# Kernel tuning notes

Hardware: AMD Instinct MI355X
Metric: run time of the kernel (lower is better)

Reference implementation:

```python
import jax, jax.numpy as jnp
import numpy as np

N_HEADS = 16
LN_EPS = 1e-5


def setup_inputs() -> dict:
    key = jax.random.key(0)
    k_z, k_qkv, k_proj = jax.random.split(key, 3)
    b, n, dm = 4, 2048, 1024
    z = jax.random.normal(k_z, (b, n, dm), dtype=jnp.float32)
    gamma = jnp.ones((dm,), dtype=jnp.float32)
    beta = jnp.zeros((dm,), dtype=jnp.float32)
    # parameterize Linear weights as (in, out) so y = x @ w (same math as torch x @ W.T)
    w_qkv = jax.random.normal(k_qkv, (dm, 3 * dm), dtype=jnp.float32) * (1.0 / np.sqrt(dm))
    w_proj = jax.random.normal(k_proj, (dm, dm), dtype=jnp.float32) * (1.0 / np.sqrt(dm))
    b_proj = jnp.zeros((dm,), dtype=jnp.float32)
    return {"z": z, "gamma": gamma, "beta": beta, "w_qkv": w_qkv,
            "w_proj": w_proj, "b_proj": b_proj}


def reference(z, gamma, beta, w_qkv, w_proj, b_proj):
    b, n, dm = z.shape
    h = N_HEADS
    d = dm // h
    scaling = jnp.asarray(np.sqrt(dm / h), dtype=z.dtype)

    # LayerNorm over last dim
    mu = jnp.mean(z, axis=-1, keepdims=True)
    var = jnp.mean(jnp.square(z - mu), axis=-1, keepdims=True)
    zn = (z - mu) * jax.lax.rsqrt(var + LN_EPS) * gamma + beta

    qkv = zn @ w_qkv  # [b, n, 3*dm]
    # einops 'b n (h d qkv_n) -> qkv_n b h n d': qkv index is INNERMOST of packed dim
    qkv = qkv.reshape(b, n, h, d, 3)
    q = qkv[..., 0]  # [b, n, h, d]
    k = qkv[..., 1]
    v = qkv[..., 2]

    scores = jnp.einsum('bqhd,bkhd->bhqk', q, k) / scaling  # [b, h, n, n]
    att = jax.nn.softmax(scores, axis=-1)
    out = jnp.einsum('bhqk,bkhd->bqhd', att, v).reshape(b, n, dm)
    out = out @ w_proj + b_proj  # projection (drop_hidden=False); dropout is identity in eval
    return z + out
```

## Files before the change

kernel.cpp:

```cpp
#include <hip/hip_runtime.h>

typedef unsigned short ushort;
typedef unsigned int uint;

typedef __bf16 bf16x8 __attribute__((ext_vector_type(8)));
typedef float floatx4 __attribute__((ext_vector_type(4)));

constexpr int BATCH = 4;
constexpr int SEQ = 2048;
constexpr int DM = 1024;
constexpr int NH = 16;
constexpr int HD = 64;
constexpr int M = BATCH * SEQ;
constexpr int NQKV = 3 * DM;
constexpr float QSCALE = 0.18033688011112042f;

__device__ __forceinline__ ushort f2b(float f) {
    uint x; __builtin_memcpy(&x, &f, 4);
    x += 0x7fffu + ((x >> 16) & 1u);
    return (ushort)(x >> 16);
}

__device__ __forceinline__ void gload16(const ushort* g, ushort* l) {
    __builtin_amdgcn_global_load_lds(
        (const __attribute__((address_space(1))) void*)g,
        (__attribute__((address_space(3))) void*)l, 16, 0, 0);
}

__global__ __launch_bounds__(256) void prep_kernel(
    const float* __restrict__ w_qkv, ushort* __restrict__ wqT,
    const float* __restrict__ w_proj, ushort* __restrict__ wpT,
    const float* __restrict__ z, const float* __restrict__ gamma,
    const float* __restrict__ beta, ushort* __restrict__ zn) {
    __shared__ ushort tile[64][65];
    int id = blockIdx.x;
    int t = threadIdx.x;
    if (id < 1024) {
        int tx = t & 63, ty = t >> 6;
        if (id < 768) {
            int bx = id % 48, by = id / 48;
            int c0 = bx * 64, r0 = by * 64;
#pragma unroll
            for (int i = 0; i < 64; i += 4)
                tile[i + ty][tx] = f2b(w_qkv[(size_t)(r0 + i + ty) * NQKV + c0 + tx]);
            __syncthreads();
#pragma unroll
            for (int i = 0; i < 64; i += 4) {
                int c = c0 + i + ty;
                int cp = (c % 3) * DM + c / 3;
                wqT[(size_t)cp * DM + r0 + tx] = tile[tx][i + ty];
            }
        } else {
            int q = id - 768;
            int c0 = (q % 16) * 64, r0 = (q / 16) * 64;
#pragma unroll
            for (int i = 0; i < 64; i += 4)
                tile[i + ty][tx] = f2b(w_proj[(size_t)(r0 + i + ty) * DM + c0 + tx]);
            __syncthreads();
#pragma unroll
            for (int i = 0; i < 64; i += 4)
                wpT[(size_t)(c0 + i + ty) * DM + r0 + tx] = tile[tx][i + ty];
        }
        return;
    }
    int row = id - 1024;
    float4 v = reinterpret_cast<const float4*>(z + (size_t)row * DM)[t];
    float s = v.x + v.y + v.z + v.w;
    float sq = v.x * v.x + v.y * v.y + v.z * v.z + v.w * v.w;
#pragma unroll
    for (int off = 32; off >= 1; off >>= 1) {
        s  += __shfl_xor(s, off);
        sq += __shfl_xor(sq, off);
    }
    __shared__ float red[8];
    int wave = t >> 6;
    if ((t & 63) == 0) { red[wave] = s; red[wave + 4] = sq; }
    __syncthreads();
    s  = red[0] + red[1] + red[2] + red[3];
    sq = red[4] + red[5] + red[6] + red[7];
    float mean = s * (1.f / DM);
    float var  = sq * (1.f / DM) - mean * mean;
    float rstd = rsqrtf(var + 1e-5f);
    float4 g = reinterpret_cast<const float4*>(gamma)[t];
    float4 bt = reinterpret_cast<const float4*>(beta)[t];
    ushort4 o;
    o.x = f2b((v.x - mean) * rstd * g.x + bt.x);
    o.y = f2b((v.y - mean) * rstd * g.y + bt.y);
    o.z = f2b((v.z - mean) * rstd * g.z + bt.z);
    o.w = f2b((v.w - mean) * rstd * g.w + bt.w);
    reinterpret_cast<ushort4*>(zn + (size_t)row * DM)[t] = o;
}

__device__ __forceinline__ void gemm128_core(
    const ushort* __restrict__ A, const ushort* __restrict__ BT,
    int m0, int n0, int t, floatx4 (&acc)[4][4],
    ushort (*As)[64], ushort (*Bs)[64]) {
    int lane = t & 63, w = t >> 6;
    int l16 = lane & 15, quad = lane >> 4;
    int wm = (w >> 1) * 64, wn = (w & 1) * 64;
#pragma unroll
    for (int i = 0; i < 4; i++)
#pragma unroll
        for (int j = 0; j < 4; j++) acc[i][j] = (floatx4){0.f, 0.f, 0.f, 0.f};

    int srow8 = lane >> 3;
    int lseg = (lane & 7) ^ srow8;
    const ushort* gA[4]; const ushort* gB[4];
    ushort* lA[4]; ushort* lB[4];
#pragma unroll
    for (int c = 0; c < 4; c++) {
        int r = 32 * c + 8 * w + srow8;
        gA[c] = &A [(size_t)(m0 + r) * DM + lseg * 8];
        gB[c] = &BT[(size_t)(n0 + r) * DM + lseg * 8];
        lA[c] = &As[32 * c + 8 * w][0];
        lB[c] = &Bs[32 * c + 8 * w][0];
    }
    int sw = l16 & 7;

    for (int k0 = 0; k0 < DM; k0 += 64) {
#pragma unroll
        for (int c = 0; c < 4; c++) {
            gload16(gA[c] + k0, lA[c]);
            gload16(gB[c] + k0, lB[c]);
        }
        __syncthreads();
#pragma unroll
        for (int kk = 0; kk < 2; kk++) {
            bf16x8 af[4], bf[4];
#pragma unroll
            for (int i = 0; i < 4; i++)
                af[i] = *reinterpret_cast<const bf16x8*>(
                    &As[wm + i * 16 + l16][((kk * 4 + quad) ^ sw) << 3]);
#pragma unroll
            for (int j = 0; j < 4; j++)
                bf[j] = *reinterpret_cast<const bf16x8*>(
                    &Bs[wn + j * 16 + l16][((kk * 4 + quad) ^ sw) << 3]);
#pragma unroll
            for (int i = 0; i < 4; i++)
#pragma unroll
                for (int j = 0; j < 4; j++)
                    acc[i][j] = __builtin_amdgcn_mfma_f32_16x16x32_bf16(
                        af[i], bf[j], acc[i][j], 0, 0, 0);
        }
        __syncthreads();
    }
}

__global__ __launch_bounds__(512) void gemm_qkv256(
    const ushort* __restrict__ A,
    const ushort* __restrict__ BT,
    ushort* __restrict__ Q, ushort* __restrict__ K, ushort* __restrict__ V) {
    __shared__ ushort smem[65536];
    int t = threadIdx.x;
    int lane = t & 63, w = t >> 6;
    int l16 = lane & 15, quad = lane >> 4;
    int wm = w >> 2, wn = w & 3;
    int id = blockIdx.x;
    int m0 = (id & 31) * 256, n0 = (id >> 5) * 256;

    int srow = t >> 3;
    int sseg = (t & 7) ^ (srow & 7);
    const ushort* gA[4]; const ushort* gB[4];
#pragma unroll
    for (int c = 0; c < 4; c++) {
        int r = c * 64 + srow;
        gA[c] = A  + (size_t)(m0 + r) * DM + sseg * 8;
        gB[c] = BT + (size_t)(n0 + r) * DM + sseg * 8;
    }
    int wbase = w * 512;

    auto stage = [&](int k0, int d) {
        int ab = d * 16384, bb2 = 32768 + d * 16384;
#pragma unroll
        for (int c = 0; c < 4; c++) {
            gload16(gA[c] + k0, &smem[ab  + c * 4096 + wbase]);
            gload16(gB[c] + k0, &smem[bb2 + c * 4096 + wbase]);
        }
    };

    floatx4 acc[8][4];
#pragma unroll
    for (int i = 0; i < 8; i++)
#pragma unroll
        for (int j = 0; j < 4; j++) acc[i][j] = (floatx4){0.f, 0.f, 0.f, 0.f};

    int sw = l16 & 7;

    stage(0, 0);
    stage(64, 1);
    for (int kt = 0; kt < 16; kt++) {
        int d = kt & 1;
        if (kt < 15)
            asm volatile("s_waitcnt vmcnt(8)\n\ts_barrier" ::: "memory");
        else
            asm volatile("s_waitcnt vmcnt(0)\n\ts_barrier" ::: "memory");
        int ab = d * 16384, bb2 = 32768 + d * 16384;
#pragma unroll
        for (int kk = 0; kk < 2; kk++) {
            bf16x8 bf[4];
#pragma unroll
            for (int j = 0; j < 4; j++)
                bf[j] = *reinterpret_cast<const bf16x8*>(
                    &smem[bb2 + (wn * 64 + j * 16 + l16) * 64 +
                          (((kk * 4 + quad) ^ sw) << 3)]);
#pragma unroll
            for (int ig = 0; ig < 2; ig++) {
                bf16x8 af[4];
#pragma unroll
                for (int ii = 0; ii < 4; ii++)
                    af[ii] = *reinterpret_cast<const bf16x8*>(
                        &smem[ab + (wm * 128 + (ig * 4 + ii) * 16 + l16) * 64 +
                              (((kk * 4 + quad) ^ sw) << 3)]);
                __builtin_amdgcn_s_setprio(1);
#pragma unroll
                for (int ii = 0; ii < 4; ii++)
#pragma unroll
                    for (int j = 0; j < 4; j++)
                        acc[ig * 4 + ii][j] = __builtin_amdgcn_mfma_f32_16x16x32_bf16(
                            af[ii], bf[j], acc[ig * 4 + ii][j], 0, 0, 0);
                __builtin_amdgcn_s_setprio(0);
            }
        }
        asm volatile("s_waitcnt lgkmcnt(0)\n\ts_barrier" ::: "memory");
        if (kt + 2 < 16) stage((kt + 2) * 64, d);
    }

    int which = n0 >> 10;
    int hd0 = n0 & 1023;
    int bbx = m0 >> 11;
    int nb = m0 & 2047;
    float scale = (which == 0) ? QSCALE : 1.0f;

    if (which < 2) {
        ushort* dst = (which == 0) ? Q : K;
#pragma unroll
        for (int p = 0; p < 2; p++) {
            if (wm == p) {
#pragma unroll
                for (int i = 0; i < 8; i++)
#pragma unroll
                    for (int j = 0; j < 4; j++)
#pragma unroll
                        for (int r = 0; r < 4; r++)
                            smem[(i * 16 + quad * 4 + r) * 264 + wn * 64 + j * 16 + l16] =
                                f2b(acc[i][j][r] * scale);
            }
            asm volatile("s_waitcnt lgkmcnt(0)\n\ts_barrier" ::: "memory");
            int ch = (t & 31) * 8;
#pragma unroll
            for (int u = 0; u < 8; u++) {
                int r = (t >> 5) + u * 16;
                int n = nb + p * 128 + r;
                int col = hd0 + ch;
                int hh = col >> 6, dd = col & 63;
                *reinterpret_cast<uint4*>(
                    &dst[((size_t)((bbx * NH + hh) * SEQ) + n) * HD + dd]) =
                    *reinterpret_cast<const uint4*>(&smem[r * 264 + ch]);
            }
            asm volatile("s_waitcnt lgkmcnt(0)\n\ts_barrier" ::: "memory");
        }
    } else {
#pragma unroll
        for (int p = 0; p < 2; p++) {
            if (wm == p) {
#pragma unroll
                for (int i = 0; i < 8; i++)
#pragma unroll
                    for (int j = 0; j < 4; j++)
#pragma unroll
                        for (int r = 0; r < 4; r++)
                            smem[(wn * 64 + j * 16 + l16) * 136 + i * 16 + quad * 4 + r] =
                                f2b(acc[i][j][r]);
            }
            asm volatile("s_waitcnt lgkmcnt(0)\n\ts_barrier" ::: "memory");
            int nch = (t & 15) * 8;
#pragma unroll
            for (int u = 0; u < 8; u++) {
                int dc = (t >> 4) + u * 32;
                int hh = (hd0 >> 6) + (dc >> 6), dd = dc & 63;
                int n = nb + p * 128 + nch;
                *reinterpret_cast<uint4*>(
                    &V[((size_t)((bbx * NH + hh) * HD) + dd) * SEQ + n]) =
                    *reinterpret_cast<const uint4*>(&smem[dc * 136 + nch]);
            }
            asm volatile("s_waitcnt lgkmcnt(0)\n\ts_barrier" ::: "memory");
        }
    }
}

__global__ __launch_bounds__(256) void gemm_proj(
    const ushort* __restrict__ A,
    const ushort* __restrict__ BT,
    const float* __restrict__ bias, const float* __restrict__ z,
    float* __restrict__ out) {
    __shared__ ushort As[128][64];
    __shared__ ushort Bs[128][64];
    int t = threadIdx.x;
    int id = blockIdx.x;
    int m0 = (id & 63) * 128, n0 = (id >> 6) * 128;
    floatx4 acc[4][4];
    gemm128_core(A, BT, m0, n0, t, acc, As, Bs);
    int lane = t & 63, w = t >> 6;
    int l16 = lane & 15, quad = lane >> 4;
    int wm = (w >> 1) * 64, wn = (w & 1) * 64;
#pragma unroll
    for (int j = 0; j < 4; j++) {
        int col = n0 + wn + j * 16 + l16;
        float bz = bias[col];
#pragma unroll
        for (int i = 0; i < 4; i++) {
#pragma unroll
            for (int r = 0; r < 4; r++) {
                int row = m0 + wm + i * 16 + quad * 4 + r;
                out[(size_t)row * DM + col] =
                    acc[i][j][r] + bz + z[(size_t)row * DM + col];
            }
        }
    }
}

__global__ __launch_bounds__(256) void attn_kernel(
    const ushort* __restrict__ Q, const ushort* __restrict__ K,
    const ushort* __restrict__ Vt, ushort* __restrict__ O) {
    __shared__ ushort QsPs[128 * 64];
    __shared__ ushort Ks[64 * 64];
    __shared__ ushort Vs[64 * 64];
    int t = threadIdx.x;
    int lane = t & 63, w = t >> 6;
    int l16 = lane & 15, quad = lane >> 4;
    int id = blockIdx.x;
    int qt = id >> 6, bh = id & 63;
    int bb = bh >> 4, h = bh & 15;
    int q0 = qt * 128;
    const ushort* Qg = Q  + (size_t)((bb * NH + h) * SEQ + q0) * HD;
    const ushort* Kg = K  + (size_t)((bb * NH + h) * SEQ) * HD;
    const ushort* Vg = Vt + (size_t)((bb * NH + h) * HD) * SEQ;

    int srow = lane >> 3;
    int lseg = (lane & 7) ^ srow;
    int r0 = 8 * w + srow;

    gload16(Qg + (size_t)r0 * HD + lseg * 8,         &QsPs[w * 512]);
    gload16(Qg + (size_t)(32 + r0) * HD + lseg * 8,  &QsPs[2048 + w * 512]);
    gload16(Qg + (size_t)(64 + r0) * HD + lseg * 8,  &QsPs[4096 + w * 512]);
    gload16(Qg + (size_t)(96 + r0) * HD + lseg * 8,  &QsPs[6144 + w * 512]);
    gload16(Kg + (size_t)r0 * HD + lseg * 8,         &Ks[w * 512]);
    gload16(Kg + (size_t)(32 + r0) * HD + lseg * 8,  &Ks[2048 + w * 512]);
    gload16(Vg + (size_t)r0 * SEQ + lseg * 8,        &Vs[w * 512]);
    gload16(Vg + (size_t)(32 + r0) * SEQ + lseg * 8, &Vs[2048 + w * 512]);
    __syncthreads();

    int swl = l16 & 7;
    bf16x8 aq[2][2];
    ushort* PsRow[2];
#pragma unroll
    for (int g = 0; g < 2; g++) {
        int row = 32 * w + 16 * g + l16;
        aq[g][0] = *reinterpret_cast<const bf16x8*>(&QsPs[row * 64 + ((quad ^ swl) << 3)]);
        aq[g][1] = *reinterpret_cast<const bf16x8*>(&QsPs[row * 64 + (((quad + 4) ^ swl) << 3)]);
        PsRow[g] = &QsPs[row * 64];
    }

    size_t koff1 = (size_t)r0 * HD + lseg * 8;
    size_t koff2 = (size_t)(32 + r0) * HD + lseg * 8;
    size_t voff1 = (size_t)r0 * SEQ + lseg * 8;
    size_t voff2 = (size_t)(32 + r0) * SEQ + lseg * 8;
    ushort* kw1 = &Ks[w * 512 + (lane & 63) * 8];
    ushort* kw2 = &Ks[2048 + w * 512 + (lane & 63) * 8];
    ushort* vw1 = &Vs[w * 512 + (lane & 63) * 8];
    ushort* vw2 = &Vs[2048 + w * 512 + (lane & 63) * 8];
    const ushort* Kp = Kg + (size_t)64 * HD;
    const ushort* Vp = Vg + 64;

    bf16x8 bones;
    {
        union { ushort u[8]; bf16x8 v; } cvt;
        ushort one = (l16 == 0) ? (ushort)0x3F80 : (ushort)0;
#pragma unroll
        for (int i = 0; i < 8; i++) cvt.u[i] = one;
        bones = cvt.v;
    }

    floatx4 Oacc[2][4], lacc[2];
#pragma unroll
    for (int g = 0; g < 2; g++) {
        lacc[g] = (floatx4){0.f, 0.f, 0.f, 0.f};
#pragma unroll
        for (int tt = 0; tt < 4; tt++) Oacc[g][tt] = (floatx4){0.f, 0.f, 0.f, 0.f};
    }

    constexpr int NT = SEQ / 64;
    for (int kt = 0; kt < NT; kt++) {
        uint4 kr1 = *reinterpret_cast<const uint4*>(Kp + koff1);
        uint4 kr2 = *reinterpret_cast<const uint4*>(Kp + koff2);
        uint4 vr1 = *reinterpret_cast<const uint4*>(Vp + voff1);
        uint4 vr2 = *reinterpret_cast<const uint4*>(Vp + voff2);
        Kp += (size_t)64 * HD;
        Vp += 64;

        floatx4 sacc[2][4];
#pragma unroll
        for (int nt = 0; nt < 4; nt++) {
            bf16x8 ak0 = *reinterpret_cast<const bf16x8*>(&Ks[(nt * 16 + l16) * 64 + ((quad ^ swl) << 3)]);
            bf16x8 ak1 = *reinterpret_cast<const bf16x8*>(&Ks[(nt * 16 + l16) * 64 + (((quad + 4) ^ swl) << 3)]);
#pragma unroll
            for (int g = 0; g < 2; g++) {
                floatx4 sv = (floatx4){0.f, 0.f, 0.f, 0.f};
                sv = __builtin_amdgcn_mfma_f32_16x16x32_bf16(ak0, aq[g][0], sv, 0, 0, 0);
                sv = __builtin_amdgcn_mfma_f32_16x16x32_bf16(ak1, aq[g][1], sv, 0, 0, 0);
                sacc[g][nt] = sv;
            }
        }
#pragma unroll
        for (int g = 0; g < 2; g++) {
#pragma unroll
            for (int nt = 0; nt < 4; nt++) {
                float p0 = __builtin_amdgcn_exp2f(sacc[g][nt][0]);
                float p1 = __builtin_amdgcn_exp2f(sacc[g][nt][1]);
                float p2 = __builtin_amdgcn_exp2f(sacc[g][nt][2]);
                float p3 = __builtin_amdgcn_exp2f(sacc[g][nt][3]);
                uint b0, b1, b2, b3;
                __builtin_memcpy(&b0, &p0, 4); __builtin_memcpy(&b1, &p1, 4);
                __builtin_memcpy(&b2, &p2, 4); __builtin_memcpy(&b3, &p3, 4);
                uint2 pk;
                pk.x = __builtin_amdgcn_perm(b1, b0, 0x07060302u);
                pk.y = __builtin_amdgcn_perm(b3, b2, 0x07060302u);
                int lseg2 = 2 * nt + (quad >> 1);
                *reinterpret_cast<uint2*>(&PsRow[g][((lseg2 ^ swl) << 3) + (quad & 1) * 4]) = pk;
            }
        }
#pragma unroll
        for (int ks = 0; ks < 2; ks++) {
            bf16x8 ap[2];
#pragma unroll
            for (int g = 0; g < 2; g++) {
                ap[g] = *reinterpret_cast<const bf16x8*>(
                    &PsRow[g][(((4 * ks + quad) ^ swl) << 3)]);
                lacc[g] = __builtin_amdgcn_mfma_f32_16x16x32_bf16(ap[g], bones, lacc[g], 0, 0, 0);
            }
#pragma unroll
            for (int tt = 0; tt < 4; tt++) {
                bf16x8 bv = *reinterpret_cast<const bf16x8*>(
                    &Vs[(tt * 16 + l16) * 64 + ((((ks * 4 + quad)) ^ swl) << 3)]);
#pragma unroll
                for (int g = 0; g < 2; g++)
                    Oacc[g][tt] = __builtin_amdgcn_mfma_f32_16x16x32_bf16(ap[g], bv, Oacc[g][tt], 0, 0, 0);
            }
        }
        __syncthreads();
        *reinterpret_cast<uint4*>(kw1) = kr1;
        *reinterpret_cast<uint4*>(kw2) = kr2;
        *reinterpret_cast<uint4*>(vw1) = vr1;
        *reinterpret_cast<uint4*>(vw2) = vr2;
        __syncthreads();
    }
    float lq[2][4];
#pragma unroll
    for (int g = 0; g < 2; g++)
#pragma unroll
        for (int j = 0; j < 4; j++) lq[g][j] = __shfl(lacc[g][j], quad << 4);

#pragma unroll
    for (int g = 0; g < 2; g++) {
#pragma unroll
        for (int tt = 0; tt < 4; tt++) {
#pragma unroll
            for (int j = 0; j < 4; j++) {
                int n = q0 + 32 * w + 16 * g + quad * 4 + j;
                int dcol = tt * 16 + l16;
                float val = Oacc[g][tt][j] / lq[g][j];
                O[(size_t)(bb * SEQ + n) * DM + h * HD + dcol] = f2b(val);
            }
        }
    }
}

extern "C" void kernel_launch(void* const* d_in, const int* in_sizes, int n_in,
                              void* d_out, int out_size, void* d_ws, size_t ws_size,
                              hipStream_t stream) {
    const float* z      = (const float*)d_in[0];
    const float* gamma  = (const float*)d_in[1];
    const float* beta   = (const float*)d_in[2];
    const float* w_qkv  = (const float*)d_in[3];
    const float* w_proj = (const float*)d_in[4];
    const float* b_proj = (const float*)d_in[5];
    float* out = (float*)d_out;

    char* ws = (char*)d_ws;
    const size_t SZ = (size_t)M * DM * sizeof(ushort);
    ushort* zn   = (ushort*)(ws);
    ushort* Qb   = (ushort*)(ws + SZ);
    ushort* Kb   = (ushort*)(ws + 2 * SZ);
    ushort* Vb   = (ushort*)(ws + 3 * SZ);
    ushort* wqT  = (ushort*)(ws + 4 * SZ);
    ushort* wpT  = (ushort*)(ws + 4 * SZ + (size_t)DM * NQKV * sizeof(ushort));
    ushort* Ob = zn;

    prep_kernel<<<1024 + M, 256, 0, stream>>>(w_qkv, wqT, w_proj, wpT,
                                              z, gamma, beta, zn);
    gemm_qkv256<<<(M / 256) * (NQKV / 256), 512, 0, stream>>>(zn, wqT, Qb, Kb, Vb);
    attn_kernel<<<(SEQ / 128) * BATCH * NH, 256, 0, stream>>>(Qb, Kb, Vb, Ob);
    gemm_proj<<<(DM / 128) * 64, 256, 0, stream>>>(Ob, wpT, b_proj, z, out);
}
```

Before: 276.4 us.

## Restructure QKV GEMM main loop into ping-pong phased schedule with prefetch depth one

The QKV GEMM main loop changes from a two-stage-ahead prefetch with coarse barriers to a one-ahead prefetch. The next tile's global loads are issued right after the first fragment reads. The MFMA work is split into four sub-phases, each separated by s_barrier and sched_barrier so that LDS reads and MFMAs from different waves interleave in a ping-pong pattern. The goal is better overlap of LDS traffic with matrix math and fewer register-held A fragments. In exchange, prefetch depth drops from two stages to one and each iteration waits on vmcnt(0), which can expose global load latency.

```diff
diff --git a/kernel.cpp b/kernel.cpp
--- a/kernel.cpp
+++ b/kernel.cpp
@@ -187,43 +187,69 @@
     int sw = l16 & 7;
 
     stage(0, 0);
-    stage(64, 1);
     for (int kt = 0; kt < 16; kt++) {
         int d = kt & 1;
-        if (kt < 15)
-            asm volatile("s_waitcnt vmcnt(8)\n\ts_barrier" ::: "memory");
-        else
-            asm volatile("s_waitcnt vmcnt(0)\n\ts_barrier" ::: "memory");
         int ab = d * 16384, bb2 = 32768 + d * 16384;
-#pragma unroll
-        for (int kk = 0; kk < 2; kk++) {
-            bf16x8 bf[4];
-#pragma unroll
-            for (int j = 0; j < 4; j++)
-                bf[j] = *reinterpret_cast<const bf16x8*>(
+
+        asm volatile("s_waitcnt vmcnt(0)" ::: "memory");
+        __builtin_amdgcn_s_barrier();
+
+        bf16x8 bf[4][2];
+#pragma unroll
+        for (int j = 0; j < 4; j++)
+#pragma unroll
+            for (int kk = 0; kk < 2; kk++)
+                bf[j][kk] = *reinterpret_cast<const bf16x8*>(
                     &smem[bb2 + (wn * 64 + j * 16 + l16) * 64 +
                           (((kk * 4 + quad) ^ sw) << 3)]);
-#pragma unroll
-            for (int ig = 0; ig < 2; ig++) {
-                bf16x8 af[4];
-#pragma unroll
-                for (int ii = 0; ii < 4; ii++)
-                    af[ii] = *reinterpret_cast<const bf16x8*>(
-                        &smem[ab + (wm * 128 + (ig * 4 + ii) * 16 + l16) * 64 +
+        bf16x8 af[2][2];
+#pragma unroll
+        for (int ii = 0; ii < 2; ii++)
+#pragma unroll
+            for (int kk = 0; kk < 2; kk++)
+                af[ii][kk] = *reinterpret_cast<const bf16x8*>(
+                    &smem[ab + (wm * 128 + ii * 16 + l16) * 64 +
+                          (((kk * 4 + quad) ^ sw) << 3)]);
+        if (kt + 1 < 16) stage((kt + 1) * 64, d ^ 1);
+        __builtin_amdgcn_s_barrier();
+        asm volatile("s_waitcnt lgkmcnt(0)" ::: "memory");
+        __builtin_amdgcn_sched_barrier(0);
+        __builtin_amdgcn_s_setprio(1);
+#pragma unroll
+        for (int ii = 0; ii < 2; ii++)
+#pragma unroll
+            for (int kk = 0; kk < 2; kk++)
+#pragma unroll
+                for (int j = 0; j < 4; j++)
+                    acc[ii][j] = __builtin_amdgcn_mfma_f32_16x16x32_bf16(
+                        af[ii][kk], bf[j][kk], acc[ii][j], 0, 0, 0);
+        __builtin_amdgcn_s_setprio(0);
+
+#pragma unroll
+        for (int p = 1; p < 4; p++) {
+#pragma unroll
+            for (int ii = 0; ii < 2; ii++)
+#pragma unroll
+                for (int kk = 0; kk < 2; kk++)
+                    af[ii][kk] = *reinterpret_cast<const bf16x8*>(
+                        &smem[ab + (wm * 128 + (2 * p + ii) * 16 + l16) * 64 +
                               (((kk * 4 + quad) ^ sw) << 3)]);
-                __builtin_amdgcn_s_setprio(1);
-#pragma unroll
-                for (int ii = 0; ii < 4; ii++)
+            __builtin_amdgcn_s_barrier();
+            asm volatile("s_waitcnt lgkmcnt(0)" ::: "memory");
+            __builtin_amdgcn_sched_barrier(0);
+            __builtin_amdgcn_s_setprio(1);
+#pragma unroll
+            for (int ii = 0; ii < 2; ii++)
+#pragma unroll
+                for (int kk = 0; kk < 2; kk++)
 #pragma unroll
                     for (int j = 0; j < 4; j++)
-                        acc[ig * 4 + ii][j] = __builtin_amdgcn_mfma_f32_16x16x32_bf16(
-                            af[ii], bf[j], acc[ig * 4 + ii][j], 0, 0, 0);
-                __builtin_amdgcn_s_setprio(0);
-            }
-        }
-        asm volatile("s_waitcnt lgkmcnt(0)\n\ts_barrier" ::: "memory");
-        if (kt + 2 < 16) stage((kt + 2) * 64, d);
-    }
+                        acc[2 * p + ii][j] = __builtin_amdgcn_mfma_f32_16x16x32_bf16(
+                            af[ii][kk], bf[j][kk], acc[2 * p + ii][j], 0, 0, 0);
+            __builtin_amdgcn_s_setprio(0);
+        }
+    }
+    asm volatile("s_waitcnt lgkmcnt(0)\n\ts_barrier" ::: "memory");
 
     int which = n0 >> 10;
     int hd0 = n0 & 1023;
```

Result: no change. 276.1 us (-0.1%).
